# Kernel optimization log

Hardware: AMD Instinct MI355X
Metric: run time of the kernel (lower is better)

## Reference

```python
import jax, jax.numpy as jnp
import numpy as np
import math

EMBED_DIM = 1024
N_HEADS = 16
HEAD_DIM = EMBED_DIM // N_HEADS
NUM_CLASSES = 1000


def setup_inputs() -> dict:
    key = jax.random.key(0)
    k_x, k_wi, k_bi, k_wo, k_bo = jax.random.split(key, 5)
    bs, seq_len = 2, 2048
    x = jax.random.normal(k_x, (bs, seq_len, EMBED_DIM), dtype=jnp.float32)
    # torch.nn.Linear default init: U(-1/sqrt(fan_in), 1/sqrt(fan_in))
    bi = 1.0 / math.sqrt(EMBED_DIM)
    W_in = jax.random.uniform(k_wi, (EMBED_DIM, EMBED_DIM), minval=-bi, maxval=bi, dtype=jnp.float32)
    b_in = jax.random.uniform(k_bi, (EMBED_DIM,), minval=-bi, maxval=bi, dtype=jnp.float32)
    W_out = jax.random.uniform(k_wo, (NUM_CLASSES, EMBED_DIM), minval=-bi, maxval=bi, dtype=jnp.float32)
    b_out = jax.random.uniform(k_bo, (NUM_CLASSES,), minval=-bi, maxval=bi, dtype=jnp.float32)
    return {"x": x, "W_in": W_in, "b_in": b_in, "W_out": W_out, "b_out": b_out}


def reference(x, W_in, b_in, W_out, b_out):
    bs, seq_len, f = x.shape
    # input projection: x @ W_in^T + b_in
    p = jnp.einsum('bsf,gf->bsg', x, W_in) + b_in           # [bs, seq, embed]
    p = p.reshape(bs, seq_len, N_HEADS, HEAD_DIM)            # [bs, seq, h, d]
    p = jnp.transpose(p, (0, 2, 1, 3))                        # [bs, h, seq, d]
    scale = 1.0 / math.sqrt(f)                                # note: sqrt(embed_dim), not head_dim
    attn = jnp.einsum('bhqd,bhkd->bhqk', p, p) * scale        # [bs, h, seq, seq], no softmax
    vals = jnp.einsum('bhqk,bhkd->bhqd', attn, p)             # [bs, h, seq, d]
    vals = jnp.transpose(vals, (0, 2, 1, 3)).reshape(bs, seq_len, f)
    out = jnp.einsum('bsf,cf->bsc', vals, W_out) + b_out      # [bs, seq, num_classes]
    return out
```

## Files before the change

kernel.cpp:

```cpp
#include <hip/hip_runtime.h>
#include <hip/hip_bf16.h>
#include <cstdint>

#define EMBED   1024
#define NHEADS  16
#define HDIM    64
#define SEQ     2048
#define BSZ     2
#define MTOT    (BSZ*SEQ)
#define NCLS    1000
#define NPAD    1024

typedef __attribute__((ext_vector_type(8))) short short8;
typedef __attribute__((ext_vector_type(4))) short short4v;
typedef __attribute__((ext_vector_type(4))) float float4v;

typedef __attribute__((address_space(3))) unsigned lds_uint;
typedef __attribute__((address_space(1))) const unsigned gbl_uint;

__device__ __forceinline__ void gl2lds16(const void* g, void* l) {
    __builtin_amdgcn_global_load_lds((gbl_uint*)g, (lds_uint*)l, 16, 0, 0);
}

#define WAITVM4() asm volatile("s_waitcnt vmcnt(4)" ::: "memory")
#define WAITVM0() asm volatile("s_waitcnt vmcnt(0)" ::: "memory")
#define BAR()     asm volatile("s_barrier" ::: "memory")

__device__ __forceinline__ void storeC(float* p, float v) { *p = v; }
__device__ __forceinline__ void storeC(__hip_bfloat16* p, float v) { *p = __float2bfloat16(v); }

__device__ __forceinline__ unsigned packbf2(float a, float b) {
    __hip_bfloat16 ha = __float2bfloat16(a), hb = __float2bfloat16(b);
    unsigned short ua, ub;
    __builtin_memcpy(&ua, &ha, 2); __builtin_memcpy(&ub, &hb, 2);
    return (unsigned)ua | ((unsigned)ub << 16);
}
__device__ __forceinline__ short8 lds8u(const __hip_bfloat16* p) {
    union { uint2 u[2]; short8 s; } v;
    v.u[0] = *(const uint2*)p;
    v.u[1] = *(const uint2*)(p + 4);
    return v.s;
}

#define XN4  ((MTOT*EMBED)/4)
#define WN4  ((EMBED*EMBED)/4)
__global__ __launch_bounds__(256)
void conv_inputs(const float* __restrict__ x, const float* __restrict__ Win,
                 __hip_bfloat16* __restrict__ xb, __hip_bfloat16* __restrict__ Winb) {
    const long i4 = (long)blockIdx.x * 256 + threadIdx.x;
    float4v v;
    __hip_bfloat16* dst;
    if (i4 < XN4) {
        v = *(const float4v*)(x + i4 * 4);
        dst = xb + i4 * 4;
    } else {
        const long j = i4 - XN4;
        v = *(const float4v*)(Win + j * 4);
        dst = Winb + j * 4;
    }
    short4v o;
#pragma unroll
    for (int u = 0; u < 4; u++)
        ((__hip_bfloat16*)&o)[u] = __float2bfloat16(v[u]);
    *(short4v*)dst = o;
}

template <typename CT>
__global__ __launch_bounds__(256, 4)
void gemm_bt_bias(const __hip_bfloat16* __restrict__ A,
                  const __hip_bfloat16* __restrict__ B,
                  const float* __restrict__ bias,
                  CT* __restrict__ C,
                  int nstore, int cstride, long bstride) {
    __shared__ __hip_bfloat16 As[2][64 * 64];
    __shared__ __hip_bfloat16 Bs[2][64 * 64];

    const int t    = threadIdx.x;
    const int blk  = blockIdx.x;
    const int xcd  = blk & 7;
    const int j    = blk >> 3;
    const int bm   = (xcd * 8 + (j & 7)) * 64;
    const int bn   = (j >> 3) * 64;
    const __hip_bfloat16* Bb = B + (long)(bm >> 11) * bstride;
    const int wave = t >> 6, lane = t & 63;
    const int wm   = (wave & 1) * 32, wn = (wave >> 1) * 32;
    const int lrow = lane & 15, lq = lane >> 4;

    const __hip_bfloat16* Arow[2];
    const __hip_bfloat16* Brow[2];
#pragma unroll
    for (int i = 0; i < 2; i++) {
        const int ci = i * 256 + t;
        const int r  = ci >> 3;
        const int sc = ((ci & 7) ^ (r & 7)) * 8;
        Arow[i] = A  + (long)(bm + r) * EMBED + sc;
        Brow[i] = Bb + (long)(bn + r) * EMBED + sc;
    }

    float4v acc[2][2];
#pragma unroll
    for (int i = 0; i < 2; i++)
#pragma unroll
        for (int jj = 0; jj < 2; jj++) acc[i][jj] = (float4v){0.f, 0.f, 0.f, 0.f};

    const int nIter = EMBED >> 6;

#define STAGE_TILE(k0, buf)                                                     \
    do {                                                                        \
        _Pragma("unroll")                                                       \
        for (int i = 0; i < 2; i++)                                             \
            gl2lds16(Arow[i] + (k0), (char*)As[buf] + (i * 256 + t) * 16);      \
        _Pragma("unroll")                                                       \
        for (int i = 0; i < 2; i++)                                             \
            gl2lds16(Brow[i] + (k0), (char*)Bs[buf] + (i * 256 + t) * 16);      \
    } while (0)

    STAGE_TILE(0, 0);

    for (int it = 0; it < nIter; ++it) {
        const int cur = it & 1, nxt = cur ^ 1;
        if (it + 1 < nIter) {
            STAGE_TILE((it + 1) << 6, nxt);
            WAITVM4();
        } else {
            WAITVM0();
        }
        BAR();

        const __hip_bfloat16* Ac = As[cur];
        const __hip_bfloat16* Bc = Bs[cur];
#pragma unroll
        for (int kk = 0; kk < 2; kk++) {
            short8 af[2], bf[2];
#pragma unroll
            for (int i = 0; i < 2; i++) {
                const int row = wm + i * 16 + lrow;
                const int sc  = (kk * 4 + lq) ^ (row & 7);
                af[i] = *(const short8*)(Ac + row * 64 + sc * 8);
            }
#pragma unroll
            for (int jj = 0; jj < 2; jj++) {
                const int row = wn + jj * 16 + lrow;
                const int sc  = (kk * 4 + lq) ^ (row & 7);
                bf[jj] = *(const short8*)(Bc + row * 64 + sc * 8);
            }
#pragma unroll
            for (int i = 0; i < 2; i++)
#pragma unroll
                for (int jj = 0; jj < 2; jj++)
                    acc[i][jj] = __builtin_amdgcn_mfma_f32_16x16x32_bf16(af[i], bf[jj], acc[i][jj], 0, 0, 0);
        }
        BAR();
    }
#undef STAGE_TILE

    float bv[2];
#pragma unroll
    for (int jj = 0; jj < 2; jj++) {
        const int gn = bn + wn + jj * 16 + lrow;
        bv[jj] = (gn < nstore) ? bias[gn] : 0.f;
    }
#pragma unroll
    for (int i = 0; i < 2; i++) {
        const int gm0 = bm + wm + i * 16 + lq * 4;
#pragma unroll
        for (int jj = 0; jj < 2; jj++) {
            const int gn = bn + wn + jj * 16 + lrow;
            if (gn < nstore) {
#pragma unroll
                for (int r = 0; r < 4; r++)
                    storeC(&C[(long)(gm0 + r) * cstride + gn], acc[i][jj][r] + bv[jj]);
            }
        }
    }
}

__global__ __launch_bounds__(256)
void gram64(const __hip_bfloat16* __restrict__ P, float* __restrict__ Gpart) {
    __shared__ __hip_bfloat16 Pt[64 * 68];
    const int t    = threadIdx.x;
    const int blk  = blockIdx.x;
    const int bh   = blk >> 1;
    const int half = blk & 1;
    const int b    = bh >> 4, h = bh & 15;
    const int row0 = b * SEQ + half * 1024;

    const int wave = t >> 6, lane = t & 63;
    const int lrow = lane & 15, lq = lane >> 4;

    float4v g4[4];
#pragma unroll
    for (int t2 = 0; t2 < 4; t2++) g4[t2] = (float4v){0.f, 0.f, 0.f, 0.f};

    for (int c = 0; c < 16; c++) {
#pragma unroll
        for (int i = 0; i < 2; i++) {
            const int ci = i * 256 + t;
            const int r = ci >> 3, c8 = (ci & 7) * 8;
            short8 v = *(const short8*)(P + (long)(row0 + c * 64 + r) * EMBED + h * HDIM + c8);
#pragma unroll
            for (int u = 0; u < 8; u++)
                Pt[(c8 + u) * 68 + r] = ((const __hip_bfloat16*)&v)[u];
        }
        __syncthreads();

#pragma unroll
        for (int k0 = 0; k0 < 64; k0 += 32) {
            short8 af = lds8u(Pt + (wave * 16 + lrow) * 68 + k0 + lq * 8);
#pragma unroll
            for (int t2 = 0; t2 < 4; t2++) {
                short8 bfr = lds8u(Pt + (t2 * 16 + lrow) * 68 + k0 + lq * 8);
                g4[t2] = __builtin_amdgcn_mfma_f32_16x16x32_bf16(af, bfr, g4[t2], 0, 0, 0);
            }
        }
        __syncthreads();
    }

    float* Gh = Gpart + (long)blk * 4096;
    const int d1b = wave * 16 + lq * 4;
#pragma unroll
    for (int t2 = 0; t2 < 4; t2++) {
        const int d2 = t2 * 16 + lrow;
#pragma unroll
        for (int r = 0; r < 4; r++)
            Gh[(d1b + r) * 64 + d2] = g4[t2][r];
    }
}

__global__ __launch_bounds__(256)
void weff_kernel(const float* __restrict__ Wout, const float* __restrict__ Gpart,
                 __hip_bfloat16* __restrict__ WeffT) {
    const int n0 = blockIdx.x * 64;
    const int h  = blockIdx.y;
    const int b  = blockIdx.z;
    const float* G0 = Gpart + (long)((b * 16 + h) * 2 + 0) * 4096;
    const float* G1 = Gpart + (long)((b * 16 + h) * 2 + 1) * 4096;

    __shared__ __hip_bfloat16 Wl[64 * 72];
    __shared__ __hip_bfloat16 Gl[64 * 72];
    const int t = threadIdx.x;

#pragma unroll
    for (int it = 0; it < 4; it++) {
        const int ci = it * 256 + t;
        const int r = ci >> 4, c4 = (ci & 15) * 4;
        float4v v = (float4v){0.f, 0.f, 0.f, 0.f};
        if (n0 + r < NCLS)
            v = *(const float4v*)(Wout + (long)(n0 + r) * EMBED + h * HDIM + c4);
        *(uint2*)(Wl + r * 72 + c4) = (uint2){packbf2(v[0], v[1]), packbf2(v[2], v[3])};
        float4v g0 = *(const float4v*)(G0 + r * 64 + c4);
        float4v g1 = *(const float4v*)(G1 + r * 64 + c4);
        *(uint2*)(Gl + r * 72 + c4) =
            (uint2){packbf2(g0[0] + g1[0], g0[1] + g1[1]),
                    packbf2(g0[2] + g1[2], g0[3] + g1[3])};
    }
    __syncthreads();

    const int wave = t >> 6, lane = t & 63;
    const int lrow = lane & 15, lq = lane >> 4;
    float4v acc[4];
#pragma unroll
    for (int jj = 0; jj < 4; jj++) acc[jj] = (float4v){0.f, 0.f, 0.f, 0.f};

#pragma unroll
    for (int k0 = 0; k0 < 64; k0 += 32) {
        short8 af = *(const short8*)(Wl + (wave * 16 + lrow) * 72 + k0 + lq * 8);
#pragma unroll
        for (int jj = 0; jj < 4; jj++) {
            short8 bfr = *(const short8*)(Gl + (jj * 16 + lrow) * 72 + k0 + lq * 8);
            acc[jj] = __builtin_amdgcn_mfma_f32_16x16x32_bf16(af, bfr, acc[jj], 0, 0, 0);
        }
    }

    const float scale = 1.0f / 32.0f;
    __hip_bfloat16* Wt = WeffT + (long)b * EMBED * NPAD;
#pragma unroll
    for (int jj = 0; jj < 4; jj++) {
        const int d1 = jj * 16 + lrow;
#pragma unroll
        for (int r = 0; r < 4; r++) {
            const int n = n0 + wave * 16 + lq * 4 + r;
            Wt[(long)n * EMBED + h * HDIM + d1] = __float2bfloat16(acc[jj][r] * scale);
        }
    }
}

extern "C" void kernel_launch(void* const* d_in, const int* in_sizes, int n_in,
                              void* d_out, int out_size, void* d_ws, size_t ws_size,
                              hipStream_t stream) {
    const float* x     = (const float*)d_in[0];
    const float* W_in  = (const float*)d_in[1];
    const float* b_in  = (const float*)d_in[2];
    const float* W_out = (const float*)d_in[3];
    const float* b_out = (const float*)d_in[4];
    float* out = (float*)d_out;

    char* ws = (char*)d_ws;
    __hip_bfloat16* xb    = (__hip_bfloat16*)(ws);
    __hip_bfloat16* Winb  = (__hip_bfloat16*)(ws + (8u  << 20));
    __hip_bfloat16* P     = (__hip_bfloat16*)(ws + (10u << 20));
    float*          Gpart = (float*)(ws + (18u << 20));
    __hip_bfloat16* WeffT = (__hip_bfloat16*)(ws + (20u << 20));

    conv_inputs<<<(XN4 + WN4) / 256, 256, 0, stream>>>(x, W_in, xb, Winb);
    gemm_bt_bias<__hip_bfloat16><<<1024, 256, 0, stream>>>(
        xb, Winb, b_in, P, NPAD, NPAD, 0);
    gram64<<<64, 256, 0, stream>>>(P, Gpart);
    weff_kernel<<<dim3(16, 16, 2), 256, 0, stream>>>(W_out, Gpart, WeffT);
    gemm_bt_bias<float><<<1024, 256, 0, stream>>>(
        P, WeffT, b_out, out, NCLS, NCLS, (long)EMBED * NPAD);
}
```

Before: 127.2 us.

## Enlarge GEMM M-tile to 128 and split gram reduction into four chunks

Doubles the GEMM block tile along M to 128 rows so each wave computes a 64x32 output block, raising MFMA work per LDS/global load and halving the grid to 512 blocks. The gram kernel now splits each head's sequence into four chunks for 128 blocks instead of 64, improving CU utilization, and the weff kernel sums four partials. Larger tiles increase register and LDS use and reduce block count, which may lower occupancy and latency hiding.

```diff
diff --git a/kernel.cpp b/kernel.cpp
--- a/kernel.cpp
+++ b/kernel.cpp
@@ -22,7 +22,7 @@
     __builtin_amdgcn_global_load_lds((gbl_uint*)g, (lds_uint*)l, 16, 0, 0);
 }
 
-#define WAITVM4() asm volatile("s_waitcnt vmcnt(4)" ::: "memory")
+#define WAITVM6() asm volatile("s_waitcnt vmcnt(6)" ::: "memory")
 #define WAITVM0() asm volatile("s_waitcnt vmcnt(0)" ::: "memory")
 #define BAR()     asm volatile("s_barrier" ::: "memory")
 
@@ -66,40 +66,46 @@
 }
 
 template <typename CT>
-__global__ __launch_bounds__(256, 4)
+__global__ __launch_bounds__(256)
 void gemm_bt_bias(const __hip_bfloat16* __restrict__ A,
                   const __hip_bfloat16* __restrict__ B,
                   const float* __restrict__ bias,
                   CT* __restrict__ C,
                   int nstore, int cstride, long bstride) {
-    __shared__ __hip_bfloat16 As[2][64 * 64];
+    __shared__ __hip_bfloat16 As[2][128 * 64];
     __shared__ __hip_bfloat16 Bs[2][64 * 64];
 
     const int t    = threadIdx.x;
     const int blk  = blockIdx.x;
     const int xcd  = blk & 7;
     const int j    = blk >> 3;
-    const int bm   = (xcd * 8 + (j & 7)) * 64;
-    const int bn   = (j >> 3) * 64;
+    const int bm   = (xcd * 4 + (j & 3)) * 128;
+    const int bn   = (j >> 2) * 64;
     const __hip_bfloat16* Bb = B + (long)(bm >> 11) * bstride;
     const int wave = t >> 6, lane = t & 63;
-    const int wm   = (wave & 1) * 32, wn = (wave >> 1) * 32;
+    const int wm   = (wave & 1) * 64, wn = (wave >> 1) * 32;
     const int lrow = lane & 15, lq = lane >> 4;
 
-    const __hip_bfloat16* Arow[2];
+    const __hip_bfloat16* Arow[4];
     const __hip_bfloat16* Brow[2];
+#pragma unroll
+    for (int i = 0; i < 4; i++) {
+        const int ci = i * 256 + t;
+        const int r  = ci >> 3;
+        const int sc = ((ci & 7) ^ (r & 7)) * 8;
+        Arow[i] = A + (long)(bm + r) * EMBED + sc;
+    }
 #pragma unroll
     for (int i = 0; i < 2; i++) {
         const int ci = i * 256 + t;
         const int r  = ci >> 3;
         const int sc = ((ci & 7) ^ (r & 7)) * 8;
-        Arow[i] = A  + (long)(bm + r) * EMBED + sc;
         Brow[i] = Bb + (long)(bn + r) * EMBED + sc;
     }
 
-    float4v acc[2][2];
-#pragma unroll
-    for (int i = 0; i < 2; i++)
+    float4v acc[4][2];
+#pragma unroll
+    for (int i = 0; i < 4; i++)
 #pragma unroll
         for (int jj = 0; jj < 2; jj++) acc[i][jj] = (float4v){0.f, 0.f, 0.f, 0.f};
 
@@ -108,7 +114,7 @@
 #define STAGE_TILE(k0, buf)                                                     \
     do {                                                                        \
         _Pragma("unroll")                                                       \
-        for (int i = 0; i < 2; i++)                                             \
+        for (int i = 0; i < 4; i++)                                             \
             gl2lds16(Arow[i] + (k0), (char*)As[buf] + (i * 256 + t) * 16);      \
         _Pragma("unroll")                                                       \
         for (int i = 0; i < 2; i++)                                             \
@@ -121,7 +127,7 @@
         const int cur = it & 1, nxt = cur ^ 1;
         if (it + 1 < nIter) {
             STAGE_TILE((it + 1) << 6, nxt);
-            WAITVM4();
+            WAITVM6();
         } else {
             WAITVM0();
         }
@@ -131,9 +137,9 @@
         const __hip_bfloat16* Bc = Bs[cur];
 #pragma unroll
         for (int kk = 0; kk < 2; kk++) {
-            short8 af[2], bf[2];
-#pragma unroll
-            for (int i = 0; i < 2; i++) {
+            short8 af[4], bf[2];
+#pragma unroll
+            for (int i = 0; i < 4; i++) {
                 const int row = wm + i * 16 + lrow;
                 const int sc  = (kk * 4 + lq) ^ (row & 7);
                 af[i] = *(const short8*)(Ac + row * 64 + sc * 8);
@@ -145,7 +151,7 @@
                 bf[jj] = *(const short8*)(Bc + row * 64 + sc * 8);
             }
 #pragma unroll
-            for (int i = 0; i < 2; i++)
+            for (int i = 0; i < 4; i++)
 #pragma unroll
                 for (int jj = 0; jj < 2; jj++)
                     acc[i][jj] = __builtin_amdgcn_mfma_f32_16x16x32_bf16(af[i], bf[jj], acc[i][jj], 0, 0, 0);
@@ -161,7 +167,7 @@
         bv[jj] = (gn < nstore) ? bias[gn] : 0.f;
     }
 #pragma unroll
-    for (int i = 0; i < 2; i++) {
+    for (int i = 0; i < 4; i++) {
         const int gm0 = bm + wm + i * 16 + lq * 4;
 #pragma unroll
         for (int jj = 0; jj < 2; jj++) {
@@ -176,14 +182,14 @@
 }
 
 __global__ __launch_bounds__(256)
-void gram64(const __hip_bfloat16* __restrict__ P, float* __restrict__ Gpart) {
+void gram128(const __hip_bfloat16* __restrict__ P, float* __restrict__ Gpart) {
     __shared__ __hip_bfloat16 Pt[64 * 68];
     const int t    = threadIdx.x;
     const int blk  = blockIdx.x;
-    const int bh   = blk >> 1;
-    const int half = blk & 1;
+    const int bh   = blk >> 2;
+    const int q    = blk & 3;
     const int b    = bh >> 4, h = bh & 15;
-    const int row0 = b * SEQ + half * 1024;
+    const int row0 = b * SEQ + q * 512;
 
     const int wave = t >> 6, lane = t & 63;
     const int lrow = lane & 15, lq = lane >> 4;
@@ -192,7 +198,7 @@
 #pragma unroll
     for (int t2 = 0; t2 < 4; t2++) g4[t2] = (float4v){0.f, 0.f, 0.f, 0.f};
 
-    for (int c = 0; c < 16; c++) {
+    for (int c = 0; c < 8; c++) {
 #pragma unroll
         for (int i = 0; i < 2; i++) {
             const int ci = i * 256 + t;
@@ -233,8 +239,10 @@
     const int n0 = blockIdx.x * 64;
     const int h  = blockIdx.y;
     const int b  = blockIdx.z;
-    const float* G0 = Gpart + (long)((b * 16 + h) * 2 + 0) * 4096;
-    const float* G1 = Gpart + (long)((b * 16 + h) * 2 + 1) * 4096;
+    const float* G0 = Gpart + (long)((b * 16 + h) * 4 + 0) * 4096;
+    const float* G1 = Gpart + (long)((b * 16 + h) * 4 + 1) * 4096;
+    const float* G2 = Gpart + (long)((b * 16 + h) * 4 + 2) * 4096;
+    const float* G3 = Gpart + (long)((b * 16 + h) * 4 + 3) * 4096;
 
     __shared__ __hip_bfloat16 Wl[64 * 72];
     __shared__ __hip_bfloat16 Gl[64 * 72];
@@ -250,9 +258,12 @@
         *(uint2*)(Wl + r * 72 + c4) = (uint2){packbf2(v[0], v[1]), packbf2(v[2], v[3])};
         float4v g0 = *(const float4v*)(G0 + r * 64 + c4);
         float4v g1 = *(const float4v*)(G1 + r * 64 + c4);
-        *(uint2*)(Gl + r * 72 + c4) =
-            (uint2){packbf2(g0[0] + g1[0], g0[1] + g1[1]),
-                    packbf2(g0[2] + g1[2], g0[3] + g1[3])};
+        float4v g2 = *(const float4v*)(G2 + r * 64 + c4);
+        float4v g3 = *(const float4v*)(G3 + r * 64 + c4);
+        float4v gs;
+#pragma unroll
+        for (int u = 0; u < 4; u++) gs[u] = ((g0[u] + g1[u]) + g2[u]) + g3[u];
+        *(uint2*)(Gl + r * 72 + c4) = (uint2){packbf2(gs[0], gs[1]), packbf2(gs[2], gs[3])};
     }
     __syncthreads();
 
@@ -303,10 +314,10 @@
     __hip_bfloat16* WeffT = (__hip_bfloat16*)(ws + (20u << 20));
 
     conv_inputs<<<(XN4 + WN4) / 256, 256, 0, stream>>>(x, W_in, xb, Winb);
-    gemm_bt_bias<__hip_bfloat16><<<1024, 256, 0, stream>>>(
+    gemm_bt_bias<__hip_bfloat16><<<512, 256, 0, stream>>>(
         xb, Winb, b_in, P, NPAD, NPAD, 0);
-    gram64<<<64, 256, 0, stream>>>(P, Gpart);
+    gram128<<<128, 256, 0, stream>>>(P, Gpart);
     weff_kernel<<<dim3(16, 16, 2), 256, 0, stream>>>(W_out, Gpart, WeffT);
-    gemm_bt_bias<float><<<1024, 256, 0, stream>>>(
+    gemm_bt_bias<float><<<512, 256, 0, stream>>>(
         P, WeffT, b_out, out, NCLS, NCLS, (long)EMBED * NPAD);
 }
```

After: 125.1 us. No clear change (-1.7%).
